# Performance work log

Hardware: AMD Instinct MI355X
Metric: run time of the kernel (lower is better)

The kernel has to match this reference:

```python
import jax, jax.numpy as jnp
import numpy as np

B, T, N_MODEL, HEAD_SIZE = 8, 4096, 1024, 128


def setup_inputs() -> dict:
    key = jax.random.key(0)
    k1, k2 = jax.random.split(key)
    x = jax.random.normal(k1, (B, T, N_MODEL), dtype=jnp.float32)
    W_K = jax.random.normal(k2, (HEAD_SIZE, N_MODEL), dtype=jnp.float32) * 0.02
    return {"x": x, "W_K": W_K}


def _rope_inplace_semantics(t, cos, sin):
    """Replicates the source's in-place slice writes:
    even' = t1*cos + t2*sin  (written first)
    odd'  = -even'*sin + t2*cos  (t1 view already holds even' when read)
    """
    t1 = t[..., ::2]
    t2 = t[..., 1::2]
    even = t1 * cos + t2 * sin
    odd = -even * sin + t2 * cos
    # re-interleave: [..., half, 2] -> [..., head_size]
    return jnp.stack([even, odd], axis=-1).reshape(t.shape)


def reference(x, W_K):
    head_size = W_K.shape[0]
    T_len = x.shape[-2]
    half = head_size // 2
    # frequency-only thetas (no position index, as in source)
    thetas = jnp.power(10000.0, -(jnp.arange(half, dtype=jnp.float32) / half))
    cos = jnp.cos(thetas)
    sin = jnp.sin(thetas)

    # NOTE: source uses self.K for k, q AND v (faithful to the bug)
    k = x @ W_K.T  # [B, T, head_size]
    v = k
    k_rot = _rope_inplace_semantics(k, cos, sin)
    q_rot = k_rot  # q computed identically from K(x)

    # w[i,j] = k_i . q_j (k first, as in source einsum)
    w = jnp.einsum('bik,bjk->bij', k_rot, q_rot) * (head_size ** -0.5)
    mask = jnp.triu(jnp.full((T_len, T_len), -jnp.inf, dtype=w.dtype), k=1)
    w = jax.nn.softmax(w + mask, axis=-1)
    out = jnp.einsum('bij,bjk->bik', w, v)  # [B, T, head_size]
    return out
```

## Files before the change

### kernel.cpp

```cpp
#include <hip/hip_runtime.h>
#include <hip/hip_bf16.h>
#include <cstdint>

typedef __attribute__((ext_vector_type(8))) __bf16 bf16x8;
typedef __attribute__((ext_vector_type(4))) float f32x4;
typedef __attribute__((ext_vector_type(16))) float f32x16;

typedef const __attribute__((address_space(1))) void* as1cvp;
typedef __attribute__((address_space(3))) void* as3vp;

__device__ __forceinline__ void gload_lds16(const void* g, void* l) {
  __builtin_amdgcn_global_load_lds((as1cvp)g, (as3vp)l, 16, 0, 0);
}
__device__ __forceinline__ float readlane_f(float v, int l) {
  return __uint_as_float((uint32_t)__builtin_amdgcn_readlane((int)__float_as_uint(v), l));
}

#define KSCALE 0.3570962f
#define SMBIAS 24.0f

__device__ __forceinline__ int vperm(int p) {
  return 16 * (p >> 4) + 4 * ((p >> 3) & 1) + 8 * ((p >> 2) & 1) + (p & 3);
}

__global__ __launch_bounds__(256) void wk_convert_kernel(
    const float* __restrict__ wk, __bf16* __restrict__ wkbf) {
  int i = (blockIdx.x * 256 + threadIdx.x) * 4;
  f32x4 v = *(const f32x4*)(wk + i);
  union { __bf16 e[4]; uint64_t u; } p;
#pragma unroll
  for (int j = 0; j < 4; j++) p.e[j] = (__bf16)v[j];
  *(uint64_t*)(wkbf + i) = p.u;
}

__global__ __launch_bounds__(256, 4) void proj_rope_kernel(
    const float* __restrict__ x, const __bf16* __restrict__ wkbf,
    __bf16* __restrict__ k2, __bf16* __restrict__ vt3)
{
  __shared__ __align__(16) char psmem[40960];
  const int tid = threadIdx.x;
  const int wid = tid >> 6;
  const int lane = tid & 63;
  const int m0 = blockIdx.x * 32;
  const int wn = wid * 32;

  f32x4 acc[2][2];
#pragma unroll
  for (int i = 0; i < 2; i++)
#pragma unroll
    for (int j = 0; j < 2; j++) acc[i][j] = (f32x4)0.f;

  const int ar = tid >> 3, ac = (tid & 7) * 8;
  const float* gx0 = x + (size_t)(m0 + ar) * 1024 + ac;

  f32x4 pa0, pa1;
#define LOADA(K0) do { const float* gp = gx0 + (K0); pa0 = *(const f32x4*)gp; pa1 = *(const f32x4*)(gp + 4); } while (0)
#define WRITEA(BUF) do { \
    bf16x8 av; \
    _Pragma("unroll") for (int jj = 0; jj < 4; jj++) { av[jj] = (__bf16)pa0[jj]; av[4 + jj] = (__bf16)pa1[jj]; } \
    *(bf16x8*)((__bf16*)psmem + (BUF) * 2048 + ar * 64 + (ac ^ ((ar & 7) << 3))) = av; \
  } while (0)
#define STAGEB(BUF, K0) do { \
    _Pragma("unroll") for (int h = 0; h < 4; h++) { \
      int Lc = tid + h * 256; int row = Lc >> 3, sp = Lc & 7; \
      gload_lds16((const char*)wkbf + row * 2048 + (K0) * 2 + ((sp ^ (row & 7)) << 4), \
                  psmem + 8192 + (BUF) * 16384 + Lc * 16); \
    } } while (0)

  LOADA(0);
  STAGEB(0, 0);
  WRITEA(0);
  __syncthreads();

  for (int t = 0; t < 16; t++) {
    const int buf = t & 1;
    const bool more = (t + 1 < 16);
    if (more) { LOADA((t + 1) * 64); STAGEB(buf ^ 1, (t + 1) * 64); }
    const __bf16* As = (const __bf16*)psmem + buf * 2048;
    const __bf16* Bs = (const __bf16*)(psmem + 8192 + buf * 16384);
#pragma unroll
    for (int kk = 0; kk < 2; kk++) {
      bf16x8 afr[2], bfr[2];
#pragma unroll
      for (int mi = 0; mi < 2; mi++) {
        int row = mi * 16 + (lane & 15);
        int col = (kk * 32 + (lane >> 4) * 8) ^ ((row & 7) << 3);
        afr[mi] = *(const bf16x8*)&As[row * 64 + col];
      }
#pragma unroll
      for (int ni = 0; ni < 2; ni++) {
        int row = wn + ni * 16 + (lane & 15);
        int col = (kk * 32 + (lane >> 4) * 8) ^ ((row & 7) << 3);
        bfr[ni] = *(const bf16x8*)&Bs[row * 64 + col];
      }
#pragma unroll
      for (int mi = 0; mi < 2; mi++)
#pragma unroll
        for (int ni = 0; ni < 2; ni++)
          acc[mi][ni] = __builtin_amdgcn_mfma_f32_16x16x32_bf16(afr[mi], bfr[ni], acc[mi][ni], 0, 0, 0);
    }
    if (more) WRITEA(buf ^ 1);
    __syncthreads();
  }

  float cosv[2], sinv[2];
#pragma unroll
  for (int ni = 0; ni < 2; ni++) {
    int d = wn + ni * 16 + (lane & 15);
    float theta = exp2f((float)(d >> 1) * -0.20762050593046014f);
    cosv[ni] = cosf(theta);
    sinv[ni] = sinf(theta);
  }
  __bf16* vl = (__bf16*)psmem;
  __bf16* kl_e = (__bf16*)(psmem + 8192);
  const bool evenlane = ((lane & 1) == 0);
#pragma unroll
  for (int mi = 0; mi < 2; mi++) {
#pragma unroll
    for (int r = 0; r < 4; r++) {
      int ml = mi * 16 + (lane >> 4) * 4 + r;
#pragma unroll
      for (int ni = 0; ni < 2; ni++) {
        float val = acc[mi][ni][r];
        int d = wn + ni * 16 + (lane & 15);
        vl[ml * 128 + d] = (__bf16)val;
        float partner = __shfl_xor(val, 1);
        float e = evenlane ? val : partner;
        float o = evenlane ? partner : val;
        float ev = e * cosv[ni] + o * sinv[ni];
        float od = -ev * sinv[ni] + o * cosv[ni];
        float kr = evenlane ? ev : od;
        kl_e[ml * 128 + (d ^ ((ml & 15) << 3))] = (__bf16)(kr * KSCALE);
      }
    }
  }
  __syncthreads();
  const size_t T = blockIdx.x;
  {
    int s = tid >> 4, kvb = tid & 15;
    __bf16* kg = k2 + T * 4096 + s * 256;
#pragma unroll
    for (int h = 0; h < 2; h++) {
      int kv = kvb + h * 16;
      bf16x8 w = *(const bf16x8*)&kl_e[kv * 128 + ((s * 8) ^ ((kv & 15) << 3))];
      *(bf16x8*)(kg + kv * 8) = w;
    }
  }
  {
    int d = tid >> 1, th = tid & 1;
    __bf16* vg = vt3 + T * 4096 + d * 8;
#pragma unroll
    for (int cc = 0; cc < 2; cc++) {
      int c = 2 * th + cc;
      bf16x8 w;
#pragma unroll
      for (int jj = 0; jj < 8; jj++)
        w[jj] = vl[vperm(c * 8 + jj) * 128 + d];
      *(bf16x8*)(vg + c * 1024) = w;
    }
  }
}

__global__ __launch_bounds__(256) void attn_kernel(
    const __bf16* __restrict__ k2, const __bf16* __restrict__ vt3,
    float* __restrict__ out)
{
  __shared__ __align__(16) char smem[33152];
  const int tid = threadIdx.x;
  const int split = tid >> 6;
  const int lane = tid & 63;
  const int lo5 = lane & 31;
  const int hi = lane >> 5;
  const int b = blockIdx.x & 7;
  const int g = (int)(blockIdx.x >> 3);
  const __bf16* kt = k2 + (size_t)b * 524288;
  const __bf16* vb = vt3 + (size_t)b * 524288;
  float* ob = out + (size_t)b * 4096 * 128;

  float* mA = (float*)smem;
  float* mB = (float*)(smem + 16384);
  float* lbuf = (float*)(smem + 32768);

#pragma unroll 1
  for (int pass = 0; pass < 2; pass++) {
    const int qt = pass ? (127 - g) : g;
    const int q0 = qt * 32;
    const int jd = qt;

    bf16x8 qf[8];
    {
      const __bf16* qp = kt + (size_t)qt * 4096 + lo5 * 8;
#pragma unroll
      for (int ks = 0; ks < 8; ks++) qf[ks] = *(const bf16x8*)(qp + (2 * ks + hi) * 256);
    }

    f32x16 acc[4];
#pragma unroll
    for (int dt = 0; dt < 4; dt++) acc[dt] = (f32x16)0.f;
    float l_r = 0.f;

    for (int j = split; j <= jd; j += 4) {
      const __bf16* kp = kt + (size_t)j * 4096 + lo5 * 8;
      const __bf16* vp = vb + (size_t)j * 4096 + lo5 * 8;
      bf16x8 kf[8];
#pragma unroll
      for (int ks = 0; ks < 8; ks++) kf[ks] = *(const bf16x8*)(kp + (2 * ks + hi) * 256);
      bf16x8 vf0[4], vf1[4];
#pragma unroll
      for (int dt = 0; dt < 4; dt++) {
        vf0[dt] = *(const bf16x8*)(vp + hi * 1024 + dt * 256);
        vf1[dt] = *(const bf16x8*)(vp + (2 + hi) * 1024 + dt * 256);
      }
      f32x16 S0 = (f32x16)(-SMBIAS), S1 = (f32x16)0.f;
      __builtin_amdgcn_s_setprio(1);
#pragma unroll
      for (int ks = 0; ks < 4; ks++)
        S0 = __builtin_amdgcn_mfma_f32_32x32x16_bf16(kf[ks], qf[ks], S0, 0, 0, 0);
#pragma unroll
      for (int ks = 4; ks < 8; ks++)
        S1 = __builtin_amdgcn_mfma_f32_32x32x16_bf16(kf[ks], qf[ks], S1, 0, 0, 0);
      __builtin_amdgcn_s_setprio(0);
      f32x16 S = S0 + S1;
      if (j == jd) {
        const int kv0 = j * 32;
#pragma unroll
        for (int r = 0; r < 16; r++) {
          int kvg = kv0 + (r & 3) + 8 * (r >> 2) + 4 * hi;
          if (kvg > q0 + lo5) S[r] = -1e30f;
        }
      }
      union U { __bf16 e[8]; bf16x8 v; };
      U pk0, pk1;
      float rs = 0.f;
#pragma unroll
      for (int jj = 0; jj < 8; jj++) { float p = exp2f(S[jj]); rs += p; pk0.e[jj] = (__bf16)p; }
#pragma unroll
      for (int jj = 0; jj < 8; jj++) { float p = exp2f(S[8 + jj]); rs += p; pk1.e[jj] = (__bf16)p; }
      l_r += rs;
      __builtin_amdgcn_s_setprio(1);
#pragma unroll
      for (int dt = 0; dt < 4; dt++)
        acc[dt] = __builtin_amdgcn_mfma_f32_32x32x16_bf16(pk0.v, vf0[dt], acc[dt], 0, 0, 0);
#pragma unroll
      for (int dt = 0; dt < 4; dt++)
        acc[dt] = __builtin_amdgcn_mfma_f32_32x32x16_bf16(pk1.v, vf1[dt], acc[dt], 0, 0, 0);
      __builtin_amdgcn_s_setprio(0);
    }
    l_r += __shfl_xor(l_r, 32);

#define ACC_TO(M) do { \
      _Pragma("unroll") for (int r = 0; r < 16; r++) { \
        int ql_ = (r & 3) + 8 * (r >> 2) + 4 * hi; \
        _Pragma("unroll") for (int dt = 0; dt < 4; dt++) (M)[ql_ * 128 + dt * 32 + lo5] = acc[dt][r]; } \
    } while (0)
#define ACC_ADD(M) do { \
      _Pragma("unroll") for (int r = 0; r < 16; r++) { \
        int ql_ = (r & 3) + 8 * (r >> 2) + 4 * hi; \
        _Pragma("unroll") for (int dt = 0; dt < 4; dt++) acc[dt][r] += (M)[ql_ * 128 + dt * 32 + lo5]; } \
    } while (0)
    if (split == 1) { ACC_TO(mA); if (lane < 32) lbuf[lane] = l_r; }
    if (split == 3) { ACC_TO(mB); if (lane < 32) lbuf[64 + lane] = l_r; }
    __syncthreads();
    if (split == 0) { ACC_ADD(mA); l_r += lbuf[lo5]; }
    if (split == 2) { ACC_ADD(mB); l_r += lbuf[64 + lo5]; }
    __syncthreads();
    if (split == 2) { ACC_TO(mA); if (lane < 32) lbuf[32 + lane] = l_r; }
    __syncthreads();
    if (split == 0) {
      ACC_ADD(mA);
      l_r += lbuf[32 + lo5];
      float invl = 1.0f / l_r;
#pragma unroll
      for (int r = 0; r < 16; r++) {
        const int rb = (r & 3) + 8 * (r >> 2);
        float ivr = hi ? readlane_f(invl, rb + 4) : readlane_f(invl, rb);
        const int ql = rb + 4 * hi;
        const size_t qg = (size_t)(q0 + ql);
#pragma unroll
        for (int dt = 0; dt < 4; dt++)
          ob[qg * 128 + dt * 32 + lo5] = acc[dt][r] * ivr;
      }
    }
    __syncthreads();
  }
}

extern "C" void kernel_launch(void* const* d_in, const int* in_sizes, int n_in,
                              void* d_out, int out_size, void* d_ws, size_t ws_size,
                              hipStream_t stream) {
  const float* x  = (const float*)d_in[0];
  const float* wk = (const float*)d_in[1];
  __bf16* k2  = (__bf16*)d_ws;
  __bf16* vt3 = k2 + (size_t)8 * 4096 * 128;
  float* out  = (float*)d_out;
  __bf16* wkbf = (__bf16*)d_out;
  wk_convert_kernel<<<128, 256, 0, stream>>>(wk, wkbf);
  proj_rope_kernel<<<1024, 256, 0, stream>>>(x, wkbf, k2, vt3);
  attn_kernel<<<512, 256, 0, stream>>>(k2, vt3, out);
}
```

Baseline: 91.56 us.

## Pair adjacent query tiles in 512-thread blocks with lockstep KV iteration

The attention kernel now runs 512 threads per block, with two groups of four waves each handling an adjacent query tile. A per-iteration barrier keeps the two groups reading the same K/V tiles at the same time, aiming for better cache reuse of shared KV data. The block count is halved and the LDS reduction buffers are doubled. The output store has an odd extra term multiplied by zero. The barrier adds synchronisation cost and makes every wave wait for the slowest one.

```diff
diff --git a/kernel.cpp b/kernel.cpp
--- a/kernel.cpp
+++ b/kernel.cpp
@@ -161,35 +161,38 @@
   }
 }
 
-__global__ __launch_bounds__(256) void attn_kernel(
+__global__ __launch_bounds__(512) void attn_kernel(
     const __bf16* __restrict__ k2, const __bf16* __restrict__ vt3,
     float* __restrict__ out)
 {
-  __shared__ __align__(16) char smem[33152];
+  __shared__ __align__(16) char smem[66432];
   const int tid = threadIdx.x;
-  const int split = tid >> 6;
+  const int wid = tid >> 6;
+  const int sub = wid >> 2;
+  const int sp = wid & 3;
   const int lane = tid & 63;
   const int lo5 = lane & 31;
   const int hi = lane >> 5;
   const int b = blockIdx.x & 7;
-  const int g = (int)(blockIdx.x >> 3);
+  const int gi = (int)(blockIdx.x >> 3);
   const __bf16* kt = k2 + (size_t)b * 524288;
   const __bf16* vb = vt3 + (size_t)b * 524288;
   float* ob = out + (size_t)b * 4096 * 128;
 
-  float* mA = (float*)smem;
-  float* mB = (float*)(smem + 16384);
-  float* lbuf = (float*)(smem + 32768);
+  float* mA = (float*)(smem + sub * 16384);
+  float* mB = (float*)(smem + 32768 + sub * 16384);
+  float* lbufS = (float*)(smem + 65536) + sub * 96;
 
 #pragma unroll 1
   for (int pass = 0; pass < 2; pass++) {
-    const int qt = pass ? (127 - g) : g;
-    const int q0 = qt * 32;
-    const int jd = qt;
+    const int G = pass ? (63 - gi) : gi;
+    const int tq = 2 * G + sub;
+    const int q0 = tq * 32;
+    const int jd = tq;
 
     bf16x8 qf[8];
     {
-      const __bf16* qp = kt + (size_t)qt * 4096 + lo5 * 8;
+      const __bf16* qp = kt + (size_t)tq * 4096 + lo5 * 8;
 #pragma unroll
       for (int ks = 0; ks < 8; ks++) qf[ks] = *(const bf16x8*)(qp + (2 * ks + hi) * 256);
     }
@@ -199,54 +202,61 @@
     for (int dt = 0; dt < 4; dt++) acc[dt] = (f32x16)0.f;
     float l_r = 0.f;
 
-    for (int j = split; j <= jd; j += 4) {
-      const __bf16* kp = kt + (size_t)j * 4096 + lo5 * 8;
-      const __bf16* vp = vb + (size_t)j * 4096 + lo5 * 8;
-      bf16x8 kf[8];
-#pragma unroll
-      for (int ks = 0; ks < 8; ks++) kf[ks] = *(const bf16x8*)(kp + (2 * ks + hi) * 256);
-      bf16x8 vf0[4], vf1[4];
-#pragma unroll
-      for (int dt = 0; dt < 4; dt++) {
-        vf0[dt] = *(const bf16x8*)(vp + hi * 1024 + dt * 256);
-        vf1[dt] = *(const bf16x8*)(vp + (2 + hi) * 1024 + dt * 256);
-      }
-      f32x16 S0 = (f32x16)(-SMBIAS), S1 = (f32x16)0.f;
-      __builtin_amdgcn_s_setprio(1);
-#pragma unroll
-      for (int ks = 0; ks < 4; ks++)
-        S0 = __builtin_amdgcn_mfma_f32_32x32x16_bf16(kf[ks], qf[ks], S0, 0, 0, 0);
-#pragma unroll
-      for (int ks = 4; ks < 8; ks++)
-        S1 = __builtin_amdgcn_mfma_f32_32x32x16_bf16(kf[ks], qf[ks], S1, 0, 0, 0);
-      __builtin_amdgcn_s_setprio(0);
-      f32x16 S = S0 + S1;
-      if (j == jd) {
-        const int kv0 = j * 32;
-#pragma unroll
-        for (int r = 0; r < 16; r++) {
-          int kvg = kv0 + (r & 3) + 8 * (r >> 2) + 4 * hi;
-          if (kvg > q0 + lo5) S[r] = -1e30f;
+    const int nIter = ((2 * G + 1) >> 2) + 1;
+    for (int it = 0; it < nIter; it++) {
+      __builtin_amdgcn_s_barrier();
+      const int j = 4 * it + sp;
+      if (j <= jd) {
+        const __bf16* kp = kt + (size_t)j * 4096 + lo5 * 8;
+        const __bf16* vp = vb + (size_t)j * 4096 + lo5 * 8;
+        bf16x8 kf[8];
+#pragma unroll
+        for (int ks = 0; ks < 8; ks++) kf[ks] = *(const bf16x8*)(kp + (2 * ks + hi) * 256);
+        bf16x8 vf0[4], vf1[4];
+#pragma unroll
+        for (int dt = 0; dt < 4; dt++) {
+          vf0[dt] = *(const bf16x8*)(vp + hi * 1024 + dt * 256);
+          vf1[dt] = *(const bf16x8*)(vp + (2 + hi) * 1024 + dt * 256);
         }
-      }
-      union U { __bf16 e[8]; bf16x8 v; };
-      U pk0, pk1;
-      float rs = 0.f;
-#pragma unroll
-      for (int jj = 0; jj < 8; jj++) { float p = exp2f(S[jj]); rs += p; pk0.e[jj] = (__bf16)p; }
-#pragma unroll
-      for (int jj = 0; jj < 8; jj++) { float p = exp2f(S[8 + jj]); rs += p; pk1.e[jj] = (__bf16)p; }
-      l_r += rs;
-      __builtin_amdgcn_s_setprio(1);
-#pragma unroll
-      for (int dt = 0; dt < 4; dt++)
-        acc[dt] = __builtin_amdgcn_mfma_f32_32x32x16_bf16(pk0.v, vf0[dt], acc[dt], 0, 0, 0);
-#pragma unroll
-      for (int dt = 0; dt < 4; dt++)
-        acc[dt] = __builtin_amdgcn_mfma_f32_32x32x16_bf16(pk1.v, vf1[dt], acc[dt], 0, 0, 0);
-      __builtin_amdgcn_s_setprio(0);
+        f32x16 S0 = (f32x16)(-SMBIAS), S1 = (f32x16)0.f;
+        __builtin_amdgcn_s_setprio(1);
+#pragma unroll
+        for (int ks = 0; ks < 4; ks++)
+          S0 = __builtin_amdgcn_mfma_f32_32x32x16_bf16(kf[ks], qf[ks], S0, 0, 0, 0);
+#pragma unroll
+        for (int ks = 4; ks < 8; ks++)
+          S1 = __builtin_amdgcn_mfma_f32_32x32x16_bf16(kf[ks], qf[ks], S1, 0, 0, 0);
+        __builtin_amdgcn_s_setprio(0);
+        f32x16 S = S0 + S1;
+        if (j == jd) {
+          const int kv0 = j * 32;
+#pragma unroll
+          for (int r = 0; r < 16; r++) {
+            int kvg = kv0 + (r & 3) + 8 * (r >> 2) + 4 * hi;
+            if (kvg > q0 + lo5) S[r] = -1e30f;
+          }
+        }
+        union U { __bf16 e[8]; bf16x8 v; };
+        U pk0, pk1;
+        float rs = 0.f;
+#pragma unroll
+        for (int jj = 0; jj < 8; jj++) { float p = exp2f(S[jj]); rs += p; pk0.e[jj] = (__bf16)p; }
+#pragma unroll
+        for (int jj = 0; jj < 8; jj++) { float p = exp2f(S[8 + jj]); rs += p; pk1.e[jj] = (__bf16)p; }
+        l_r += rs;
+        __builtin_amdgcn_s_setprio(1);
+#pragma unroll
+        for (int dt = 0; dt < 4; dt++)
+          acc[dt] = __builtin_amdgcn_mfma_f32_32x32x16_bf16(pk0.v, vf0[dt], acc[dt], 0, 0, 0);
+#pragma unroll
+        for (int dt = 0; dt < 4; dt++)
+          acc[dt] = __builtin_amdgcn_mfma_f32_32x32x16_bf16(pk1.v, vf1[dt], acc[dt], 0, 0, 0);
+        __builtin_amdgcn_s_setprio(0);
+      }
     }
     l_r += __shfl_xor(l_r, 32);
+
+    __syncthreads();
 
 #define ACC_TO(M) do { \
       _Pragma("unroll") for (int r = 0; r < 16; r++) { \
@@ -258,17 +268,17 @@
         int ql_ = (r & 3) + 8 * (r >> 2) + 4 * hi; \
         _Pragma("unroll") for (int dt = 0; dt < 4; dt++) acc[dt][r] += (M)[ql_ * 128 + dt * 32 + lo5]; } \
     } while (0)
-    if (split == 1) { ACC_TO(mA); if (lane < 32) lbuf[lane] = l_r; }
-    if (split == 3) { ACC_TO(mB); if (lane < 32) lbuf[64 + lane] = l_r; }
-    __syncthreads();
-    if (split == 0) { ACC_ADD(mA); l_r += lbuf[lo5]; }
-    if (split == 2) { ACC_ADD(mB); l_r += lbuf[64 + lo5]; }
-    __syncthreads();
-    if (split == 2) { ACC_TO(mA); if (lane < 32) lbuf[32 + lane] = l_r; }
-    __syncthreads();
-    if (split == 0) {
+    if (sp == 1) { ACC_TO(mA); if (lane < 32) lbufS[lane] = l_r; }
+    if (sp == 3) { ACC_TO(mB); if (lane < 32) lbufS[64 + lane] = l_r; }
+    __syncthreads();
+    if (sp == 0) { ACC_ADD(mA); l_r += lbufS[lo5]; }
+    if (sp == 2) { ACC_ADD(mB); l_r += lbufS[64 + lo5]; }
+    __syncthreads();
+    if (sp == 2) { ACC_TO(mA); if (lane < 32) lbufS[32 + lane] = l_r; }
+    __syncthreads();
+    if (sp == 0) {
       ACC_ADD(mA);
-      l_r += lbuf[32 + lo5];
+      l_r += lbufS[32 + lo5];
       float invl = 1.0f / l_r;
 #pragma unroll
       for (int r = 0; r < 16; r++) {
@@ -278,7 +288,7 @@
         const size_t qg = (size_t)(q0 + ql);
 #pragma unroll
         for (int dt = 0; dt < 4; dt++)
-          ob[qg * 128 + dt * 32 + lo5] = acc[dt][r] * ivr;
+          ob[qg * 128 + dt * 32 + lo5] = acc[dt][r] * invl * 0.f + acc[dt][r] * ivr;
       }
     }
     __syncthreads();
@@ -296,5 +306,5 @@
   __bf16* wkbf = (__bf16*)d_out;
   wk_convert_kernel<<<128, 256, 0, stream>>>(wk, wkbf);
   proj_rope_kernel<<<1024, 256, 0, stream>>>(x, wkbf, k2, vt3);
-  attn_kernel<<<512, 256, 0, stream>>>(k2, vt3, out);
-}
+  attn_kernel<<<256, 512, 0, stream>>>(k2, vt3, out);
+}
```

Measured after the change: 94.85 us. 1.04x slower.
